# Optimization experiments

Hardware: AMD Instinct MI355X
Metric: run time of the kernel (lower is better)

## Reference

```python
import jax, jax.numpy as jnp
import numpy as np
from jax import lax

B, N_SITES, FEAT, BOND, OUT = 2048, 128, 64, 32, 256
CORE_SCALE = 0.02  # keeps the 128-step matrix product finite


def setup_inputs() -> dict:
    key = jax.random.key(0)
    ks = jax.random.split(key, 6)
    return {
        "x": jax.random.normal(ks[0], (B, N_SITES, FEAT), dtype=jnp.float32),
        "cores": jax.random.normal(ks[1], (N_SITES, BOND, FEAT, BOND), dtype=jnp.float32) * CORE_SCALE,
        "start": jax.random.normal(ks[2], (1, BOND), dtype=jnp.float32),
        "end": jax.random.normal(ks[3], (BOND, 1), dtype=jnp.float32),
        "fc_w": jax.random.normal(ks[4], (OUT, 1), dtype=jnp.float32),
        "fc_b": jax.random.normal(ks[5], (OUT,), dtype=jnp.float32),
    }


def reference(x, cores, start, end, fc_w, fc_b):
    # x: [B, N, F]; cores: [N, D, F, D]; start: [1, D]; end: [D, 1]
    b = x.shape[0]
    res0 = jnp.broadcast_to(start, (b, start.shape[1]))  # [B, D]

    def step(res, site):
        xi, core = site  # xi: [B, F], core: [D, F, D]
        m = jnp.einsum('bf,dfr->bdr', xi, core)  # per-site transfer matrix [B, D, D]
        return jnp.einsum('bd,bdr->br', res, m), None

    res, _ = lax.scan(step, res0, (jnp.swapaxes(x, 0, 1), cores))
    val = res @ end  # [B, 1]
    return val @ fc_w.T + fc_b  # [B, OUT]
```

## Files before the change

### kernel.cpp

```cpp
#include <hip/hip_runtime.h>


#define NSITES 128
#define FEATD  64
#define BOND   32
#define OUTD   256
#define BT     16
#define SEGLEN 32
#define NSEG   (NSITES / SEGLEN)
#define NBT    (2048 / BT)

#define MS_RS  648
#define MS_BS  40

typedef __attribute__((ext_vector_type(4)))  float float4v;
typedef __attribute__((ext_vector_type(16))) float float16v;

__device__ __forceinline__ unsigned pk4_fp8(float a, float b, float c, float d) {
    int v = __builtin_amdgcn_cvt_pk_fp8_f32(a, b, 0, false);
    v = __builtin_amdgcn_cvt_pk_fp8_f32(c, d, v, true);
    return (unsigned)v;
}
__device__ __forceinline__ long mklong(int lo, int hi) {
    return ((long)(unsigned)lo) | (((long)hi) << 32);
}

__global__ __launch_bounds__(256)
void prep_cores8(const float* __restrict__ cores, unsigned char* __restrict__ core8) {
    __shared__ float tile[FEATD][BOND + 4];
    const int nd = blockIdx.x;
    const int t  = threadIdx.x;
    const float* src = cores + (size_t)nd * (FEATD * BOND);
    {
        int base = t * 8;
        int f = base >> 5, r0 = base & 31;
        float4 v0 = *(const float4*)(src + base);
        float4 v1 = *(const float4*)(src + base + 4);
        tile[f][r0 + 0] = v0.x; tile[f][r0 + 1] = v0.y;
        tile[f][r0 + 2] = v0.z; tile[f][r0 + 3] = v0.w;
        tile[f][r0 + 4] = v1.x; tile[f][r0 + 5] = v1.y;
        tile[f][r0 + 6] = v1.z; tile[f][r0 + 7] = v1.w;
    }
    __syncthreads();
    const int r = t >> 3, f0 = (t & 7) * 8;
    const float s = 16.0f;
    unsigned lo = pk4_fp8(tile[f0 + 0][r] * s, tile[f0 + 1][r] * s,
                          tile[f0 + 2][r] * s, tile[f0 + 3][r] * s);
    unsigned hi = pk4_fp8(tile[f0 + 4][r] * s, tile[f0 + 5][r] * s,
                          tile[f0 + 6][r] * s, tile[f0 + 7][r] * s);
    uint2 w; w.x = lo; w.y = hi;
    *(uint2*)(core8 + ((size_t)nd * BOND + r) * FEATD + f0) = w;
}

__global__ __launch_bounds__(512, 4)
void mps_seg(const float* __restrict__ x, const unsigned char* __restrict__ core8,
             unsigned char* __restrict__ Pout) {
    __shared__ __align__(16) unsigned char MS[BOND * MS_RS];
    __shared__ __align__(16) unsigned char XS[BT * 72];

    const int t    = threadIdx.x;
    const int wave = t >> 6;
    const int lane = t & 63;
    const int cl   = lane & 15;
    const int q    = lane >> 4;
    const int l    = lane & 31;
    const int h    = lane >> 5;
    const int b0   = blockIdx.x * BT;
    const int seg  = blockIdx.y;

    int pq[2][4];
    {
        int g0 = l >> 3;
        int hm = ((l >> 2) & 1) == h;
#pragma unroll
        for (int bi = 0; bi < 2; ++bi)
#pragma unroll
            for (int g = 0; g < 4; ++g)
                pq[bi][g] = (g == g0 && hm) ? (0x58 << ((l & 3) * 8)) : 0;
    }
    const int paddr = (lane ^ 32) << 2;

    const int xb = t >> 5, xf = (t & 31) * 2;
    {
        float2 x0 = *(const float2*)(x + ((size_t)(b0 + xb) * NSITES + seg * SEGLEN) * FEATD + xf);
        int v = __builtin_amdgcn_cvt_pk_fp8_f32(x0.x, x0.y, 0, false);
        *(unsigned short*)&XS[xb * 72 + xf] = (unsigned short)(v & 0xffff);
    }
    const unsigned afoff = (unsigned)((wave * 128 + cl) * FEATD + q * 8);
    long af[16];
    {
        const unsigned char* p0 = core8 + (size_t)(seg * SEGLEN) * (1024 * FEATD) + afoff;
#pragma unroll
        for (int i = 0; i < 8; ++i) {
            af[i * 2 + 0] = *(const long*)(p0 + i * (16 * FEATD));
            af[i * 2 + 1] = *(const long*)(p0 + i * (16 * FEATD) + 32);
        }
    }

    for (int k = 0; k < SEGLEN; ++k) {
        const int n = seg * SEGLEN + k;
        __syncthreads();

        long bx0 = *(const long*)&XS[cl * 72 + q * 8];
        long bx1 = *(const long*)&XS[cl * 72 + 32 + q * 8];
        float4v acc[8];
#pragma unroll
        for (int i = 0; i < 8; ++i) {
            float4v z = {0.f, 0.f, 0.f, 0.f};
            z = __builtin_amdgcn_mfma_f32_16x16x32_fp8_fp8(af[i * 2 + 0], bx0, z, 0, 0, 0);
            acc[i] = __builtin_amdgcn_mfma_f32_16x16x32_fp8_fp8(af[i * 2 + 1], bx1, z, 0, 0, 0);
        }
#pragma unroll
        for (int p = 0; p < 2; ++p)
#pragma unroll
            for (int g = 0; g < 4; ++g) {
                unsigned w = pk4_fp8(acc[p][g], acc[p + 2][g], acc[p + 4][g], acc[p + 6][g]);
                *(unsigned*)&MS[(16 * p + 4 * q + g) * MS_RS + cl * MS_BS + wave * 4] = w;
            }

        __syncthreads();

        float2 xn;
        if (k + 1 < SEGLEN) {
            xn = *(const float2*)(x + ((size_t)(b0 + xb) * NSITES + n + 1) * FEATD + xf);
            const unsigned char* p1 = core8 + (size_t)(n + 1) * (1024 * FEATD) + afoff;
#pragma unroll
            for (int i = 0; i < 8; ++i) {
                af[i * 2 + 0] = *(const long*)(p1 + i * (16 * FEATD));
                af[i * 2 + 1] = *(const long*)(p1 + i * (16 * FEATD) + 32);
            }
        }

#pragma unroll
        for (int bi = 0; bi < 2; ++bi) {
            const int bb = wave * 2 + bi;
            long a0 = *(const long*)&MS[l * MS_RS + bb * MS_BS + 8 * h];
            long a1 = *(const long*)&MS[l * MS_RS + bb * MS_BS + 16 + 8 * h];
            int x0 = __builtin_amdgcn_ds_bpermute(paddr, pq[bi][0]);
            int x1 = __builtin_amdgcn_ds_bpermute(paddr, pq[bi][1]);
            int x2 = __builtin_amdgcn_ds_bpermute(paddr, pq[bi][2]);
            int x3 = __builtin_amdgcn_ds_bpermute(paddr, pq[bi][3]);
            long bf0 = h ? mklong(x1, pq[bi][1]) : mklong(pq[bi][0], x0);
            long bf1 = h ? mklong(x3, pq[bi][3]) : mklong(pq[bi][2], x2);
            float16v pc;
#pragma unroll
            for (int i = 0; i < 16; ++i) pc[i] = 0.f;
            pc = __builtin_amdgcn_mfma_f32_32x32x16_fp8_fp8(a0, bf0, pc, 0, 0, 0);
            pc = __builtin_amdgcn_mfma_f32_32x32x16_fp8_fp8(a1, bf1, pc, 0, 0, 0);
#pragma unroll
            for (int g = 0; g < 4; ++g)
                pq[bi][g] = (int)pk4_fp8(pc[4 * g + 0] * 0.0625f, pc[4 * g + 1] * 0.0625f,
                                         pc[4 * g + 2] * 0.0625f, pc[4 * g + 3] * 0.0625f);
        }

        if (k + 1 < SEGLEN) {
            int v = __builtin_amdgcn_cvt_pk_fp8_f32(xn.x, xn.y, 0, false);
            *(unsigned short*)&XS[xb * 72 + xf] = (unsigned short)(v & 0xffff);
        }
    }

#pragma unroll
    for (int bi = 0; bi < 2; ++bi) {
        const int bb = wave * 2 + bi;
        unsigned char* gp = Pout + (((size_t)seg * 2048 + b0 + bb) * 1024);
#pragma unroll
        for (int g = 0; g < 4; ++g)
            *(unsigned*)(gp + l * 32 + 8 * g + 4 * h) = (unsigned)pq[bi][g];
    }
}

__global__ __launch_bounds__(512)
void combine(const unsigned char* __restrict__ Pout, const float* __restrict__ startv,
             const float* __restrict__ endv, const float* __restrict__ fc_w,
             const float* __restrict__ fc_b, float* __restrict__ out) {
    const int t    = threadIdx.x;
    const int wave = t >> 6;
    const int lane = t & 63;
    const int r    = lane >> 1;
    const int dh   = lane & 1;
    const int b    = blockIdx.x * 8 + wave;

    float res = startv[r];
    const unsigned char* base = Pout + (size_t)b * 1024 + dh * 512 + r;

    unsigned char by[16];
#pragma unroll
    for (int di = 0; di < 16; ++di) by[di] = base[di * 32];

    for (int s = 0; s < NSEG; ++s) {
        unsigned char by2[16];
        if (s + 1 < NSEG) {
            const unsigned char* nb = base + (size_t)(s + 1) * 2048 * 1024;
#pragma unroll
            for (int di = 0; di < 16; ++di) by2[di] = nb[di * 32];
        }
        float acc = 0.f;
#pragma unroll
        for (int di = 0; di < 16; ++di) {
            float rv = __shfl(res, dh * 32 + di * 2, 64);
            acc += rv * __builtin_amdgcn_cvt_f32_fp8((int)by[di], 0);
        }
        float tot = acc + __shfl_xor(acc, 1, 64);
        res = tot * 0.0625f;
        if (s + 1 < NSEG) {
#pragma unroll
            for (int di = 0; di < 16; ++di) by[di] = by2[di];
        }
    }

    float v = dh ? 0.f : res * endv[r];
#pragma unroll
    for (int off = 1; off < 64; off <<= 1) v += __shfl_xor(v, off, 64);

    const int j = lane * 4;
    float4 w4  = *(const float4*)(fc_w + j);
    float4 bb4 = *(const float4*)(fc_b + j);
    float4 o;
    o.x = v * w4.x + bb4.x;
    o.y = v * w4.y + bb4.y;
    o.z = v * w4.z + bb4.z;
    o.w = v * w4.w + bb4.w;
    *(float4*)(out + (size_t)b * OUTD + j) = o;
}

extern "C" void kernel_launch(void* const* d_in, const int* in_sizes, int n_in,
                              void* d_out, int out_size, void* d_ws, size_t ws_size,
                              hipStream_t stream) {
    const float* x      = (const float*)d_in[0];
    const float* cores  = (const float*)d_in[1];
    const float* startv = (const float*)d_in[2];
    const float* endv   = (const float*)d_in[3];
    const float* fc_w   = (const float*)d_in[4];
    const float* fc_b   = (const float*)d_in[5];
    float* out = (float*)d_out;

    unsigned char* core8 = (unsigned char*)d_ws;
    unsigned char* Pout  = core8 + (size_t)NSITES * 1024 * FEATD;

    prep_cores8<<<NSITES * BOND, 256, 0, stream>>>(cores, core8);
    mps_seg<<<dim3(NBT, NSEG), 512, 0, stream>>>(x, core8, Pout);
    combine<<<2048 / 8, 512, 0, stream>>>(Pout, startv, endv, fc_w, fc_b, out);
}
```

Before: 253.0 us.

## Software-pipeline transfer-matrix build with chain product via double-buffered LDS; restage combine

The segment kernel now double-buffers the per-site transfer matrix and x tiles in LDS. Site k's matrix is built while the chain product for site k-1 runs, so each step needs one barrier instead of two and the MFMA build overlaps the dependent product. The combine kernel is rewritten to stage each 16-row batch of segment products through LDS with coalesced 16-byte loads, and it keeps the running vector in shared memory instead of doing byte-wise strided global loads. The cost is doubled LDS for the segment kernel, which may reduce occupancy at the requested 4 blocks per CU.

```diff
diff --git a/kernel.cpp b/kernel.cpp
--- a/kernel.cpp
+++ b/kernel.cpp
@@ -52,11 +52,37 @@
     *(uint2*)(core8 + ((size_t)nd * BOND + r) * FEATD + f0) = w;
 }
 
+__device__ __forceinline__ void product_step(const unsigned char* __restrict__ MSb,
+                                             int pq[2][4], int wave, int l, int h,
+                                             int paddr) {
+#pragma unroll
+    for (int bi = 0; bi < 2; ++bi) {
+        const int bb = wave * 2 + bi;
+        long a0 = *(const long*)&MSb[l * MS_RS + bb * MS_BS + 8 * h];
+        long a1 = *(const long*)&MSb[l * MS_RS + bb * MS_BS + 16 + 8 * h];
+        int x0 = __builtin_amdgcn_ds_bpermute(paddr, pq[bi][0]);
+        int x1 = __builtin_amdgcn_ds_bpermute(paddr, pq[bi][1]);
+        int x2 = __builtin_amdgcn_ds_bpermute(paddr, pq[bi][2]);
+        int x3 = __builtin_amdgcn_ds_bpermute(paddr, pq[bi][3]);
+        long bf0 = h ? mklong(x1, pq[bi][1]) : mklong(pq[bi][0], x0);
+        long bf1 = h ? mklong(x3, pq[bi][3]) : mklong(pq[bi][2], x2);
+        float16v pc;
+#pragma unroll
+        for (int i = 0; i < 16; ++i) pc[i] = 0.f;
+        pc = __builtin_amdgcn_mfma_f32_32x32x16_fp8_fp8(a0, bf0, pc, 0, 0, 0);
+        pc = __builtin_amdgcn_mfma_f32_32x32x16_fp8_fp8(a1, bf1, pc, 0, 0, 0);
+#pragma unroll
+        for (int g = 0; g < 4; ++g)
+            pq[bi][g] = (int)pk4_fp8(pc[4 * g + 0] * 0.0625f, pc[4 * g + 1] * 0.0625f,
+                                     pc[4 * g + 2] * 0.0625f, pc[4 * g + 3] * 0.0625f);
+    }
+}
+
 __global__ __launch_bounds__(512, 4)
 void mps_seg(const float* __restrict__ x, const unsigned char* __restrict__ core8,
              unsigned char* __restrict__ Pout) {
-    __shared__ __align__(16) unsigned char MS[BOND * MS_RS];
-    __shared__ __align__(16) unsigned char XS[BT * 72];
+    __shared__ __align__(16) unsigned char MS[2][BOND * MS_RS];
+    __shared__ __align__(16) unsigned char XS[2][BT * 72];
 
     const int t    = threadIdx.x;
     const int wave = t >> 6;
@@ -67,6 +93,7 @@
     const int h    = lane >> 5;
     const int b0   = blockIdx.x * BT;
     const int seg  = blockIdx.y;
+    const int n0   = seg * SEGLEN;
 
     int pq[2][4];
     {
@@ -81,48 +108,55 @@
     const int paddr = (lane ^ 32) << 2;
 
     const int xb = t >> 5, xf = (t & 31) * 2;
-    {
-        float2 x0 = *(const float2*)(x + ((size_t)(b0 + xb) * NSITES + seg * SEGLEN) * FEATD + xf);
+    const unsigned afoff = (unsigned)((wave * 128 + cl) * FEATD + q * 8);
+
+    {
+        float2 x0 = *(const float2*)(x + ((size_t)(b0 + xb) * NSITES + n0) * FEATD + xf);
         int v = __builtin_amdgcn_cvt_pk_fp8_f32(x0.x, x0.y, 0, false);
-        *(unsigned short*)&XS[xb * 72 + xf] = (unsigned short)(v & 0xffff);
-    }
-    const unsigned afoff = (unsigned)((wave * 128 + cl) * FEATD + q * 8);
+        *(unsigned short*)&XS[0][xb * 72 + xf] = (unsigned short)(v & 0xffff);
+    }
+    float2 xr = *(const float2*)(x + ((size_t)(b0 + xb) * NSITES + n0 + 1) * FEATD + xf);
     long af[16];
     {
-        const unsigned char* p0 = core8 + (size_t)(seg * SEGLEN) * (1024 * FEATD) + afoff;
+        const unsigned char* p0 = core8 + (size_t)n0 * (1024 * FEATD) + afoff;
 #pragma unroll
         for (int i = 0; i < 8; ++i) {
             af[i * 2 + 0] = *(const long*)(p0 + i * (16 * FEATD));
             af[i * 2 + 1] = *(const long*)(p0 + i * (16 * FEATD) + 32);
         }
     }
+    __syncthreads();
 
     for (int k = 0; k < SEGLEN; ++k) {
-        const int n = seg * SEGLEN + k;
-        __syncthreads();
-
-        long bx0 = *(const long*)&XS[cl * 72 + q * 8];
-        long bx1 = *(const long*)&XS[cl * 72 + 32 + q * 8];
-        float4v acc[8];
-#pragma unroll
-        for (int i = 0; i < 8; ++i) {
-            float4v z = {0.f, 0.f, 0.f, 0.f};
-            z = __builtin_amdgcn_mfma_f32_16x16x32_fp8_fp8(af[i * 2 + 0], bx0, z, 0, 0, 0);
-            acc[i] = __builtin_amdgcn_mfma_f32_16x16x32_fp8_fp8(af[i * 2 + 1], bx1, z, 0, 0, 0);
-        }
-#pragma unroll
-        for (int p = 0; p < 2; ++p)
+        const int par = k & 1;
+        const int n = n0 + k;
+
+        if (k + 1 < SEGLEN) {
+            int v = __builtin_amdgcn_cvt_pk_fp8_f32(xr.x, xr.y, 0, false);
+            *(unsigned short*)&XS[par ^ 1][xb * 72 + xf] = (unsigned short)(v & 0xffff);
+        }
+        if (k + 2 < SEGLEN)
+            xr = *(const float2*)(x + ((size_t)(b0 + xb) * NSITES + n + 2) * FEATD + xf);
+
+        long bx0 = *(const long*)&XS[par][cl * 72 + q * 8];
+        long bx1 = *(const long*)&XS[par][cl * 72 + 32 + q * 8];
+#pragma unroll
+        for (int p = 0; p < 2; ++p) {
+            float4v acc[4];
+#pragma unroll
+            for (int u = 0; u < 4; ++u) {
+                float4v z = {0.f, 0.f, 0.f, 0.f};
+                z = __builtin_amdgcn_mfma_f32_16x16x32_fp8_fp8(af[(2 * u + p) * 2], bx0, z, 0, 0, 0);
+                acc[u] = __builtin_amdgcn_mfma_f32_16x16x32_fp8_fp8(af[(2 * u + p) * 2 + 1], bx1, z, 0, 0, 0);
+            }
 #pragma unroll
             for (int g = 0; g < 4; ++g) {
-                unsigned w = pk4_fp8(acc[p][g], acc[p + 2][g], acc[p + 4][g], acc[p + 6][g]);
-                *(unsigned*)&MS[(16 * p + 4 * q + g) * MS_RS + cl * MS_BS + wave * 4] = w;
+                unsigned w = pk4_fp8(acc[0][g], acc[1][g], acc[2][g], acc[3][g]);
+                *(unsigned*)&MS[par][(16 * p + 4 * q + g) * MS_RS + cl * MS_BS + wave * 4] = w;
             }
-
-        __syncthreads();
-
-        float2 xn;
+        }
+
         if (k + 1 < SEGLEN) {
-            xn = *(const float2*)(x + ((size_t)(b0 + xb) * NSITES + n + 1) * FEATD + xf);
             const unsigned char* p1 = core8 + (size_t)(n + 1) * (1024 * FEATD) + afoff;
 #pragma unroll
             for (int i = 0; i < 8; ++i) {
@@ -131,33 +165,11 @@
             }
         }
 
-#pragma unroll
-        for (int bi = 0; bi < 2; ++bi) {
-            const int bb = wave * 2 + bi;
-            long a0 = *(const long*)&MS[l * MS_RS + bb * MS_BS + 8 * h];
-            long a1 = *(const long*)&MS[l * MS_RS + bb * MS_BS + 16 + 8 * h];
-            int x0 = __builtin_amdgcn_ds_bpermute(paddr, pq[bi][0]);
-            int x1 = __builtin_amdgcn_ds_bpermute(paddr, pq[bi][1]);
-            int x2 = __builtin_amdgcn_ds_bpermute(paddr, pq[bi][2]);
-            int x3 = __builtin_amdgcn_ds_bpermute(paddr, pq[bi][3]);
-            long bf0 = h ? mklong(x1, pq[bi][1]) : mklong(pq[bi][0], x0);
-            long bf1 = h ? mklong(x3, pq[bi][3]) : mklong(pq[bi][2], x2);
-            float16v pc;
-#pragma unroll
-            for (int i = 0; i < 16; ++i) pc[i] = 0.f;
-            pc = __builtin_amdgcn_mfma_f32_32x32x16_fp8_fp8(a0, bf0, pc, 0, 0, 0);
-            pc = __builtin_amdgcn_mfma_f32_32x32x16_fp8_fp8(a1, bf1, pc, 0, 0, 0);
-#pragma unroll
-            for (int g = 0; g < 4; ++g)
-                pq[bi][g] = (int)pk4_fp8(pc[4 * g + 0] * 0.0625f, pc[4 * g + 1] * 0.0625f,
-                                         pc[4 * g + 2] * 0.0625f, pc[4 * g + 3] * 0.0625f);
-        }
-
-        if (k + 1 < SEGLEN) {
-            int v = __builtin_amdgcn_cvt_pk_fp8_f32(xn.x, xn.y, 0, false);
-            *(unsigned short*)&XS[xb * 72 + xf] = (unsigned short)(v & 0xffff);
-        }
-    }
+        if (k > 0) product_step(MS[par ^ 1], pq, wave, l, h, paddr);
+
+        __syncthreads();
+    }
+    product_step(MS[(SEGLEN - 1) & 1], pq, wave, l, h, paddr);
 
 #pragma unroll
     for (int bi = 0; bi < 2; ++bi) {
@@ -169,58 +181,62 @@
     }
 }
 
-__global__ __launch_bounds__(512)
+__global__ __launch_bounds__(256)
 void combine(const unsigned char* __restrict__ Pout, const float* __restrict__ startv,
              const float* __restrict__ endv, const float* __restrict__ fc_w,
              const float* __restrict__ fc_b, float* __restrict__ out) {
-    const int t    = threadIdx.x;
-    const int wave = t >> 6;
-    const int lane = t & 63;
-    const int r    = lane >> 1;
-    const int dh   = lane & 1;
-    const int b    = blockIdx.x * 8 + wave;
-
-    float res = startv[r];
-    const unsigned char* base = Pout + (size_t)b * 1024 + dh * 512 + r;
-
-    unsigned char by[16];
-#pragma unroll
-    for (int di = 0; di < 16; ++di) by[di] = base[di * 32];
+    __shared__ __align__(16) unsigned char st[16 * 1024];
+    __shared__ float resA[16][34], resB[16][34];
+    __shared__ float val_lds[16];
+    const int t  = threadIdx.x;
+    const int b0 = blockIdx.x * 16;
+    const int bt = t >> 4;
+    const int c  = t & 15;
+
+    for (int e = t; e < 512; e += 256) resA[e >> 5][e & 31] = startv[e & 31];
 
     for (int s = 0; s < NSEG; ++s) {
-        unsigned char by2[16];
-        if (s + 1 < NSEG) {
-            const unsigned char* nb = base + (size_t)(s + 1) * 2048 * 1024;
-#pragma unroll
-            for (int di = 0; di < 16; ++di) by2[di] = nb[di * 32];
-        }
-        float acc = 0.f;
-#pragma unroll
-        for (int di = 0; di < 16; ++di) {
-            float rv = __shfl(res, dh * 32 + di * 2, 64);
-            acc += rv * __builtin_amdgcn_cvt_f32_fp8((int)by[di], 0);
-        }
-        float tot = acc + __shfl_xor(acc, 1, 64);
-        res = tot * 0.0625f;
-        if (s + 1 < NSEG) {
-#pragma unroll
-            for (int di = 0; di < 16; ++di) by[di] = by2[di];
-        }
-    }
-
-    float v = dh ? 0.f : res * endv[r];
-#pragma unroll
-    for (int off = 1; off < 64; off <<= 1) v += __shfl_xor(v, off, 64);
-
-    const int j = lane * 4;
-    float4 w4  = *(const float4*)(fc_w + j);
-    float4 bb4 = *(const float4*)(fc_b + j);
-    float4 o;
-    o.x = v * w4.x + bb4.x;
-    o.y = v * w4.y + bb4.y;
-    o.z = v * w4.z + bb4.z;
-    o.w = v * w4.w + bb4.w;
-    *(float4*)(out + (size_t)b * OUTD + j) = o;
+        {
+            const uint4* g = (const uint4*)(Pout + ((size_t)s * 2048 + b0) * 1024);
+#pragma unroll
+            for (int it = 0; it < 4; ++it)
+                *(uint4*)&st[(it * 256 + t) * 16] = g[it * 256 + t];
+        }
+        __syncthreads();
+        const float* rin = (s & 1) ? &resB[bt][0] : &resA[bt][0];
+        float* rout      = (s & 1) ? &resA[bt][0] : &resB[bt][0];
+        float a0 = 0.f, a1 = 0.f;
+#pragma unroll
+        for (int alpha = 0; alpha < BOND; ++alpha) {
+            float rv = rin[alpha];
+            unsigned short pp = *(const unsigned short*)&st[bt * 1024 + alpha * 32 + 2 * c];
+            a0 += rv * __builtin_amdgcn_cvt_f32_fp8((int)(pp & 0xff), 0);
+            a1 += rv * __builtin_amdgcn_cvt_f32_fp8((int)(pp >> 8), 0);
+        }
+        rout[2 * c]     = a0 * 0.0625f;
+        rout[2 * c + 1] = a1 * 0.0625f;
+        __syncthreads();
+    }
+
+    float pv = resA[bt][2 * c] * endv[2 * c] + resA[bt][2 * c + 1] * endv[2 * c + 1];
+#pragma unroll
+    for (int off = 1; off < 16; off <<= 1) pv += __shfl_xor(pv, off, 64);
+    if (c == 0) val_lds[bt] = pv;
+    __syncthreads();
+
+    const float v = val_lds[bt];
+#pragma unroll
+    for (int i = 0; i < 4; ++i) {
+        int j = c * 4 + i * 64;
+        float4 w4  = *(const float4*)(fc_w + j);
+        float4 bb4 = *(const float4*)(fc_b + j);
+        float4 o;
+        o.x = v * w4.x + bb4.x;
+        o.y = v * w4.y + bb4.y;
+        o.z = v * w4.z + bb4.z;
+        o.w = v * w4.w + bb4.w;
+        *(float4*)(out + (size_t)(b0 + bt) * OUTD + j) = o;
+    }
 }
 
 extern "C" void kernel_launch(void* const* d_in, const int* in_sizes, int n_in,
@@ -239,5 +255,5 @@
 
     prep_cores8<<<NSITES * BOND, 256, 0, stream>>>(cores, core8);
     mps_seg<<<dim3(NBT, NSEG), 512, 0, stream>>>(x, core8, Pout);
-    combine<<<2048 / 8, 512, 0, stream>>>(Pout, startv, endv, fc_w, fc_b, out);
-}
+    combine<<<2048 / 16, 256, 0, stream>>>(Pout, startv, endv, fc_w, fc_b, out);
+}
```

New measurement: 245.4 us. -3.0%, faster.
